# Optimization experiments

Hardware: AMD Instinct MI355X
Metric: run time of the kernel (lower is better)

Reference implementation:

```python
import jax, jax.numpy as jnp
import numpy as np

B, C, H, W = 64, 256, 14, 14
K = 9
HID = 256   # EdgeAgg hidden_channels = in_channels
OUT = 512   # out_channels = 2*in_channels (required by final reshape)


def _knn(q, kset, k):
    # ViG dense_knn_matrix: squared-distance knn, top-k of -dist (self-loop may be included)
    qs = jnp.sum(q * q, -1)
    ks = jnp.sum(kset * kset, -1)
    dist = qs[:, :, None] - 2.0 * jnp.einsum('bnc,bmc->bnm', q, kset) + ks[:, None, :]
    _, idx = jax.lax.top_k(-dist, k)   # (B,N,k) neighbor indices into kset
    return idx


def _edgeconv_add(feat, nbr, validf, w, b):
    # PyG EdgeConv(nn=Linear, aggr='add') with per-node valid-edge mask:
    #   out[i] = sum_{j in valid nbrs(i)} cat(x_i, x_j - x_i) @ w + b
    # nn is linear, so aggregate neighbor diffs BEFORE the matmul (same math, less traffic).
    Cf = feat.shape[-1]
    wa, wb = w[:Cf], w[Cf:]
    deg = jnp.sum(validf, -1, keepdims=True)                   # (B,N,1)
    xj = feat[jnp.arange(feat.shape[0])[:, None, None], nbr]   # (B,N,k,C) gather
    sum_xj = jnp.einsum('bnkc,bnk->bnc', xj, validf)
    return deg * (feat @ wa + b) + (sum_xj - deg * feat) @ wb


def _forward(x, fc1_w, fc1_b, fc2_w, fc2_b, fce_w, fce_b, inout_w, inout_b,
             attn_w, attn_b, upd_w, upd_b, kp_w, kp_b, enc_w, enc_b,
             mu_w, mu_b, dec_w, dec_b, T):
    k = dec_w.shape[-1]
    b_, c_, h_, w_ = x.shape
    n = h_ * w_
    xs = x.reshape(b_, c_, n)                       # (B,C,N)
    x_sp = jnp.transpose(xs, (0, 2, 1))             # (B,N,C) true spatial node feats for knn
    x_sp_d = jax.lax.stop_gradient(x_sp)            # original detaches before knn
    x_nbr = _knn(x_sp_d, x_sp_d, k)
    # temporal roll across the T frames of each clip
    y_sp = jnp.roll(x_sp.reshape(b_ // T, T, n, c_), -1, axis=1).reshape(b_, n, c_)
    y_nbr = _knn(x_sp_d, jax.lax.stop_gradient(y_sp), k)
    # faithful to original: x.view(B*N, C) reinterprets the contiguous (B,C,N) buffer
    x_feat = xs.reshape(b_, n, c_)
    y_feat = jnp.transpose(y_sp, (0, 2, 1)).reshape(b_, n, c_)
    # VAE-like K predictor (deterministic z = mu); argmax -> per-node degree in [0,k)
    hk = x_feat.reshape(b_ * n, c_) @ kp_w + kp_b
    hk = jax.nn.relu(hk @ enc_w + enc_b)
    mu = hk @ mu_w + mu_b
    logits = mu @ dec_w + dec_b                     # (B*N, k)
    k_int = jnp.argmax(logits, axis=1)
    # generate_mask: keep the first k_int[i] of node i's k edges
    validf = (jnp.arange(k)[None, :] < k_int[:, None]).astype(x.dtype).reshape(b_, n, k)

    def edge_agg(feat, nbr):
        h1 = jax.nn.relu(_edgeconv_add(feat, nbr, validf, fc1_w, fc1_b))
        h2 = _edgeconv_add(h1, nbr, validf, fc2_w, fc2_b)
        return (h2 @ fce_w + fce_b).reshape(b_ * n, -1)

    x_agg = edge_agg(x_feat, x_nbr)
    y_agg = edge_agg(y_feat, y_nbr)
    scores = (jnp.concatenate([x_agg, y_agg], -1) @ attn_w + attn_b)[:, 0]
    wgt = jax.nn.softmax(scores, axis=0)[:, None]   # softmax over ALL B*N nodes (as in source)
    fused = wgt * x_agg + (1.0 - wgt) * y_agg
    xin = x_feat.reshape(b_ * n, c_) @ inout_w + inout_b
    upd = jax.nn.relu(jnp.concatenate([xin, fused], -1) @ upd_w + upd_b)   # (B*N, 2C)
    return jnp.transpose(upd.reshape(b_, n, 2 * c_), (0, 2, 1)).reshape(b_, 2 * c_, h_, w_)


def setup_inputs():
    key = jax.random.key(0)
    ks = iter(jax.random.split(key, 32))

    def lin(i, o):
        return jax.random.normal(next(ks), (i, o), jnp.float32) / np.sqrt(i)

    def bias(o):
        return jax.random.normal(next(ks), (o,), jnp.float32) * 0.01

    return {
        'x': jax.random.normal(next(ks), (B, C, H, W), jnp.float32),
        'fc1_w': lin(2 * C, HID), 'fc1_b': bias(HID),
        'fc2_w': lin(2 * HID, HID), 'fc2_b': bias(HID),
        'fce_w': lin(HID, OUT), 'fce_b': bias(OUT),
        'inout_w': lin(C, OUT), 'inout_b': bias(OUT),
        'attn_w': lin(2 * OUT, 1), 'attn_b': bias(1),
        'upd_w': lin(2 * OUT, OUT), 'upd_b': bias(OUT),
        'kp_w': lin(C, 500), 'kp_b': bias(500),
        'enc_w': lin(500, 64), 'enc_b': bias(64),
        'mu_w': lin(64, 32), 'mu_b': bias(32),
        'dec_w': lin(32, K), 'dec_b': bias(K),
        'T': 16,
    }


def reference(x, fc1_w, fc1_b, fc2_w, fc2_b, fce_w, fce_b, inout_w, inout_b,
              attn_w, attn_b, upd_w, upd_b, kp_w, kp_b, enc_w, enc_b,
              mu_w, mu_b, dec_w, dec_b, T):
    return _forward(x, fc1_w, fc1_b, fc2_w, fc2_b, fce_w, fce_b, inout_w, inout_b,
                    attn_w, attn_b, upd_w, upd_b, kp_w, kp_b, enc_w, enc_b,
                    mu_w, mu_b, dec_w, dec_b, T)
```

## Files before the change

kernel.cpp:

```cpp
#include <hip/hip_runtime.h>
#include <cstddef>
#include <cstdint>

constexpr int BATCH = 64;
constexpr int CH    = 256;
constexpr int NPT   = 196;
constexpr int ROWS  = BATCH * NPT;
constexpr int BSTRIDE = CH * NPT;
constexpr int KNB   = 8;
constexpr int DSTR  = 208;

typedef __bf16 bf16x8 __attribute__((ext_vector_type(8)));
typedef __bf16 bf16x4 __attribute__((ext_vector_type(4)));
typedef _Float16 f16x8 __attribute__((ext_vector_type(8)));
typedef float  f32x4  __attribute__((ext_vector_type(4)));
typedef unsigned long long u64;

__device__ __forceinline__ int src_batch(int b) {
    return (b & ~15) | ((b + 1) & 15);
}

__device__ __forceinline__ void gload_lds16(const void* g, void* l) {
    __builtin_amdgcn_global_load_lds(
        (const __attribute__((address_space(1))) void*)g,
        (__attribute__((address_space(3))) void*)l, 16, 0, 0);
}

__device__ __forceinline__ int xcd_swz(int lin, int nwg) {
    int q = nwg >> 3;
    return (lin & 7) * q + (lin >> 3);
}

__global__ __launch_bounds__(256) void front_kernel(const float* __restrict__ x,
        _Float16* __restrict__ XH, _Float16* __restrict__ XL,
        __bf16* __restrict__ XB, float* __restrict__ qs,
        const float* __restrict__ fc1_w, const float* __restrict__ fc2_w,
        const float* __restrict__ fce_w, const float* __restrict__ upd_w,
        const float* __restrict__ kp_w, const float* __restrict__ kp_b,
        const float* __restrict__ enc_w, const float* __restrict__ enc_b,
        const float* __restrict__ mu_w, const float* __restrict__ mu_b,
        const float* __restrict__ dec_w, const float* __restrict__ dec_b,
        const float* __restrict__ inout_w, const float* __restrict__ inout_b,
        const float* __restrict__ upd_b,
        __bf16* __restrict__ W1catT, __bf16* __restrict__ W2catT,
        __bf16* __restrict__ fcet, __bf16* __restrict__ updC,
        float* __restrict__ KW1, float* __restrict__ kb1,
        float* __restrict__ KW2, float* __restrict__ kb2,
        float* __restrict__ bcomp, int* __restrict__ smcnt) {
    __shared__ __attribute__((aligned(16))) char smem[16896];
    float (*tile)[65] = (float(*)[65])smem;
    int bid = blockIdx.x;
    int t = threadIdx.x;
    if (bid < 1024) {
        int m0 = (bid & 3) * 64, c0 = ((bid >> 2) & 3) * 64, b = bid >> 4;
        const float* xb = x + (size_t)b * BSTRIDE;
        #pragma unroll
        for (int s = 0; s < 16; ++s) {
            int idx = s * 256 + t;
            int cc = idx >> 6, mm = idx & 63;
            int m = m0 + mm;
            float v = (m < NPT) ? xb[(size_t)(c0 + cc) * NPT + m] : 0.f;
            tile[cc][mm] = v;
            if (m < NPT)
                XB[(size_t)b * BSTRIDE + (size_t)(c0 + cc) * NPT + m] = (__bf16)v;
        }
        __syncthreads();
        #pragma unroll
        for (int s = 0; s < 16; ++s) {
            int idx = s * 256 + t;
            int mm = idx >> 6, cc = idx & 63;
            float v = tile[cc][mm];
            _Float16 h = (_Float16)v;
            size_t off = ((size_t)b * 256 + (m0 + mm)) * 256 + c0 + cc;
            XH[off] = h;
            XL[off] = (_Float16)(v - (float)h);
        }
    } else if (bid < 1088) {
        int b = bid - 1024;
        int m = t;
        if (m >= NPT) return;
        const float* xb = x + (size_t)b * BSTRIDE;
        float acc = 0.f;
        for (int c = 0; c < CH; ++c) {
            float v = xb[c * NPT + m];
            acc = fmaf(v, v, acc);
        }
        qs[b * NPT + m] = acc;
    } else {
        int pbid = bid - 1088;
        if (pbid == 0 && t == 0) smcnt[0] = 0;
        if (pbid < 64) {
            const float* W = (pbid < 32) ? fc1_w : fc2_w;
            __bf16* WT = (pbid < 32) ? W1catT : W2catT;
            int local = pbid & 31;
            int n0 = (local >> 2) * 64, k0 = (local & 3) * 64;
            #pragma unroll
            for (int s = 0; s < 16; ++s) {
                int idx = s * 256 + t;
                int kk = idx >> 6, nn = idx & 63;
                float v;
                if (n0 < 256)
                    v = W[(size_t)(k0 + kk) * 256 + n0 + nn] -
                        W[(size_t)(k0 + kk + 256) * 256 + n0 + nn];
                else
                    v = W[(size_t)(k0 + kk + 256) * 256 + (n0 - 256) + nn];
                tile[kk][nn] = v;
            }
            __syncthreads();
            #pragma unroll
            for (int s = 0; s < 16; ++s) {
                int idx = s * 256 + t;
                int nn = idx >> 6, kk = idx & 63;
                WT[(size_t)(n0 + nn) * 256 + k0 + kk] = (__bf16)tile[kk][nn];
            }
        } else if (pbid < 96) {
            int local = pbid - 64;
            int n0 = (local >> 2) * 64, k0 = (local & 3) * 64;
            #pragma unroll
            for (int s = 0; s < 16; ++s) {
                int idx = s * 256 + t;
                int kk = idx >> 6, nn = idx & 63;
                tile[kk][nn] = fce_w[(size_t)(k0 + kk) * 512 + n0 + nn];
            }
            __syncthreads();
            #pragma unroll
            for (int s = 0; s < 16; ++s) {
                int idx = s * 256 + t;
                int nn = idx >> 6, kk = idx & 63;
                fcet[(size_t)(n0 + nn) * 256 + k0 + kk] = (__bf16)tile[kk][nn];
            }
        } else if (pbid < 160) {
            int local = pbid - 96;
            int k0 = (local >> 3) * 64, n0 = (local & 7) * 64;
            #pragma unroll
            for (int s = 0; s < 16; ++s) {
                int idx = s * 256 + t;
                int kk = idx >> 6, nn = idx & 63;
                tile[kk][nn] = upd_w[(size_t)(512 + k0 + kk) * 512 + n0 + nn];
            }
            __syncthreads();
            #pragma unroll
            for (int s = 0; s < 16; ++s) {
                int idx = s * 256 + t;
                int nn = idx >> 6, kk = idx & 63;
                updC[(size_t)(n0 + nn) * 768 + 256 + k0 + kk] = (__bf16)tile[kk][nn];
            }
        } else if (pbid < 224) {
            int i = (pbid - 160) * 4 + (t >> 6);
            int j = t & 63;
            double acc = 0.0;
            for (int k = 0; k < 500; ++k)
                acc += (double)kp_w[(size_t)i * 500 + k] * (double)enc_w[(size_t)k * 64 + j];
            KW1[i * 64 + j] = (float)acc;
        } else if (pbid == 224) {
            int j = t;
            if (j < 64) {
                double acc = (double)enc_b[j];
                for (int k = 0; k < 500; ++k)
                    acc += (double)kp_b[k] * (double)enc_w[(size_t)k * 64 + j];
                kb1[j] = (float)acc;
            }
        } else if (pbid < 228) {
            int e = (pbid - 225) * 256 + t;
            if (e < 576) {
                int i = e / 9, j = e - (e / 9) * 9;
                double acc = 0.0;
                for (int k = 0; k < 32; ++k)
                    acc += (double)mu_w[(size_t)i * 32 + k] * (double)dec_w[(size_t)k * 9 + j];
                KW2[e] = (float)acc;
            } else if (e < 585) {
                int j = e - 576;
                double acc = (double)dec_b[j];
                for (int k = 0; k < 32; ++k)
                    acc += (double)mu_b[k] * (double)dec_w[(size_t)k * 9 + j];
                kb2[j] = (float)acc;
            }
        } else if (pbid < 356) {
            int k0 = (pbid - 228) * 2;
            int n = t;
            double a00 = 0.0, a01 = 0.0, a10 = 0.0, a11 = 0.0;
            const float* iw0 = inout_w + (size_t)k0 * 512;
            const float* iw1 = iw0 + 512;
            for (int j = 0; j < 512; ++j) {
                double u0 = (double)upd_w[(size_t)j * 512 + n];
                double u1 = (double)upd_w[(size_t)j * 512 + n + 256];
                double w0 = (double)iw0[j];
                double w1 = (double)iw1[j];
                a00 += w0 * u0; a01 += w0 * u1;
                a10 += w1 * u0; a11 += w1 * u1;
            }
            updC[(size_t)n * 768 + k0]           = (__bf16)(float)a00;
            updC[(size_t)(n + 256) * 768 + k0]   = (__bf16)(float)a01;
            updC[(size_t)n * 768 + k0 + 1]       = (__bf16)(float)a10;
            updC[(size_t)(n + 256) * 768 + k0 + 1] = (__bf16)(float)a11;
        } else {
            int n = (pbid - 356) * 256 + t;
            double acc = (double)upd_b[n];
            for (int j = 0; j < 512; ++j)
                acc += (double)inout_b[j] * (double)upd_w[(size_t)j * 512 + n];
            bcomp[n] = (float)acc;
        }
    }
}

__global__ __launch_bounds__(256) void gram_kint(const _Float16* __restrict__ XH,
        const _Float16* __restrict__ XL, const float* __restrict__ qs,
        float* __restrict__ Dw, const float* __restrict__ x,
        const float* __restrict__ W1, const float* __restrict__ b1,
        const float* __restrict__ W2, const float* __restrict__ b2,
        int* __restrict__ kint, float* __restrict__ degf) {
    __shared__ __attribute__((aligned(16))) char smem[21056];
    int bid = blockIdx.x;
    int t = threadIdx.x;
    if (bid < 2048) {
        _Float16* Ah = (_Float16*)smem;
        _Float16* Al = Ah + 2048;
        _Float16* Bh = Al + 2048;
        _Float16* Bl = Bh + 2048;
        int nid = xcd_swz(bid, 2048);
        int job = nid >> 4;
        int tile = nid & 15;
        int by = tile >> 2, bx = tile & 3;
        int r0 = by * 64, c0 = bx * 64;
        int qb = (job < 64) ? job : job - 64;
        int kb = (job < 64) ? qb : src_batch(qb);
        int w = t >> 6, l = t & 63;
        int lr = l & 15, lg = l >> 4;
        int wr = (w >> 1) * 32, wc = (w & 1) * 32;
        const _Float16* qh = XH + (size_t)qb * 65536;
        const _Float16* ql = XL + (size_t)qb * 65536;
        const _Float16* kh = XH + (size_t)kb * 65536;
        const _Float16* kl = XL + (size_t)kb * 65536;
        f32x4 acc[2][2] = {};
        for (int k0 = 0; k0 < 256; k0 += 32) {
            {
                int row = w * 16 + (l >> 2);
                int cb = (l & 3) * 8;
                size_t goA = (size_t)(r0 + row) * 256 + k0 + cb;
                size_t goB = (size_t)(c0 + row) * 256 + k0 + cb;
                gload_lds16(qh + goA, Ah + w * 512);
                gload_lds16(ql + goA, Al + w * 512);
                gload_lds16(kh + goB, Bh + w * 512);
                gload_lds16(kl + goB, Bl + w * 512);
            }
            asm volatile("s_waitcnt vmcnt(0)" ::: "memory");
            __syncthreads();
            f16x8 ah[2], alv[2], bh[2], blv[2];
            #pragma unroll
            for (int mi = 0; mi < 2; ++mi) {
                ah[mi]  = *(const f16x8*)(Ah + (wr + mi * 16 + lr) * 32 + lg * 8);
                alv[mi] = *(const f16x8*)(Al + (wr + mi * 16 + lr) * 32 + lg * 8);
            }
            #pragma unroll
            for (int ni = 0; ni < 2; ++ni) {
                bh[ni]  = *(const f16x8*)(Bh + (wc + ni * 16 + lr) * 32 + lg * 8);
                blv[ni] = *(const f16x8*)(Bl + (wc + ni * 16 + lr) * 32 + lg * 8);
            }
            #pragma unroll
            for (int mi = 0; mi < 2; ++mi)
                #pragma unroll
                for (int ni = 0; ni < 2; ++ni) {
                    acc[mi][ni] = __builtin_amdgcn_mfma_f32_16x16x32_f16(
                        ah[mi], bh[ni], acc[mi][ni], 0, 0, 0);
                    acc[mi][ni] = __builtin_amdgcn_mfma_f32_16x16x32_f16(
                        ah[mi], blv[ni], acc[mi][ni], 0, 0, 0);
                    acc[mi][ni] = __builtin_amdgcn_mfma_f32_16x16x32_f16(
                        alv[mi], bh[ni], acc[mi][ni], 0, 0, 0);
                }
            __syncthreads();
        }
        const float* qsq = qs + qb * NPT;
        const float* qsk = qs + kb * NPT;
        float ksv[2];
        #pragma unroll
        for (int ni = 0; ni < 2; ++ni) {
            int col = c0 + wc + ni * 16 + lr;
            ksv[ni] = (col < NPT) ? qsk[col] : 0.f;
        }
        #pragma unroll
        for (int mi = 0; mi < 2; ++mi) {
            #pragma unroll
            for (int r = 0; r < 4; ++r) {
                if (r0 + wr + mi * 16 + r >= NPT) continue;
                int grow = r0 + wr + mi * 16 + lg * 4 + r;
                if (grow >= NPT) continue;
                float qq = qsq[grow];
                size_t rbase = ((size_t)job * NPT + grow) * DSTR;
                #pragma unroll
                for (int ni = 0; ni < 2; ++ni) {
                    int col = c0 + wc + ni * 16 + lr;
                    if (col < NPT)
                        Dw[rbase + col] = qq - 2.f * acc[mi][ni][r] + ksv[ni];
                }
            }
        }
    } else {
        float (*xr)[256] = (float(*)[256])smem;
        float (*ebuf)[64] = (float(*)[64])(smem + 16384);
        float (*lg2)[9]  = (float(*)[9])(smem + 20480);
        int r0 = (bid - 2048) * 16;
        const float4* xg = (const float4*)(x + (size_t)r0 * 256);
        float4* xs = (float4*)&xr[0][0];
        #pragma unroll
        for (int s = 0; s < 4; ++s) xs[s * 256 + t] = xg[s * 256 + t];
        __syncthreads();
        int w = t >> 6, l = t & 63;
        {
            float bb = b1[l];
            float a0 = bb, a1 = bb, a2 = bb, a3 = bb;
            const float* x0 = xr[w * 4 + 0];
            const float* x1 = xr[w * 4 + 1];
            const float* x2 = xr[w * 4 + 2];
            const float* x3 = xr[w * 4 + 3];
            for (int c = 0; c < 256; ++c) {
                float wv = W1[c * 64 + l];
                a0 = fmaf(x0[c], wv, a0);
                a1 = fmaf(x1[c], wv, a1);
                a2 = fmaf(x2[c], wv, a2);
                a3 = fmaf(x3[c], wv, a3);
            }
            ebuf[w * 4 + 0][l] = fmaxf(a0, 0.f);
            ebuf[w * 4 + 1][l] = fmaxf(a1, 0.f);
            ebuf[w * 4 + 2][l] = fmaxf(a2, 0.f);
            ebuf[w * 4 + 3][l] = fmaxf(a3, 0.f);
        }
        __syncthreads();
        int rr = t >> 4, cc = t & 15;
        if (cc < 9) {
            float acc = b2[cc];
            for (int j = 0; j < 64; ++j)
                acc = fmaf(ebuf[rr][j], W2[j * 9 + cc], acc);
            lg2[rr][cc] = acc;
        }
        __syncthreads();
        if (cc == 0) {
            float best = lg2[rr][0];
            int bi = 0;
            #pragma unroll
            for (int j = 1; j < 9; ++j)
                if (lg2[rr][j] > best) { best = lg2[rr][j]; bi = j; }
            kint[r0 + rr] = bi;
            degf[r0 + rr] = (float)bi;
        }
    }
}

__global__ __launch_bounds__(256) void topk_p1(const float* __restrict__ Dw,
        int* __restrict__ nbr, const __bf16* __restrict__ XB,
        const __bf16* __restrict__ W1catT, __bf16* __restrict__ P1) {
    __shared__ __attribute__((aligned(16))) char smem[32768];
    int bid = blockIdx.x;
    int t = threadIdx.x;
    if (bid < 392) {
        u64 (*lists)[4][8] = (u64(*)[4][8])smem;
        int lrow = t >> 2, q = t & 3;
        int rowid = bid * 64 + lrow;
        const float* rp = Dw + (size_t)rowid * DSTR + q * 52;
        u64 kreg[8];
        #pragma unroll
        for (int p = 0; p < 8; ++p) kreg[p] = ~0ull;
        for (int s4 = 0; s4 < 13; ++s4) {
            f32x4 dv = *(const f32x4*)(rp + s4 * 4);
            #pragma unroll
            for (int e = 0; e < 4; ++e) {
                int col = q * 52 + s4 * 4 + e;
                unsigned u = __float_as_uint(dv[e]);
                u = (u & 0x80000000u) ? ~u : (u | 0x80000000u);
                u64 key = (col < NPT) ? (((u64)u << 32) | (unsigned)col) : ~0ull;
                if (key < kreg[7]) {
                    #pragma unroll
                    for (int p = 0; p < 8; ++p) {
                        u64 mn = (key < kreg[p]) ? key : kreg[p];
                        u64 mx = (key < kreg[p]) ? kreg[p] : key;
                        kreg[p] = mn; key = mx;
                    }
                }
            }
        }
        #pragma unroll
        for (int p = 0; p < 8; ++p) lists[lrow][q][p] = kreg[p];
        __syncthreads();
        if (q == 0) {
            const u64* c = &lists[lrow][0][0];
            int p0 = 0, p1 = 0, p2 = 0, p3 = 0;
            #pragma unroll
            for (int it = 0; it < 8; ++it) {
                u64 v0 = c[p0], v1 = c[8 + p1], v2 = c[16 + p2], v3 = c[24 + p3];
                u64 best = v0; int bj = 0;
                if (v1 < best) { best = v1; bj = 1; }
                if (v2 < best) { best = v2; bj = 2; }
                if (v3 < best) { best = v3; bj = 3; }
                if (bj == 0) p0 = (p0 < 7) ? p0 + 1 : 7;
                else if (bj == 1) p1 = (p1 < 7) ? p1 + 1 : 7;
                else if (bj == 2) p2 = (p2 < 7) ? p2 + 1 : 7;
                else p3 = (p3 < 7) ? p3 + 1 : 7;
                nbr[(size_t)rowid * KNB + it] = (int)(best & 0xffffffffu);
            }
        }
    } else {
        __bf16* As = (__bf16*)smem;
        __bf16* Bs = As + 128 * 64;
        int lin = bid - 392;
        int nid = xcd_swz(lin, 392);
        int bx = nid & 3, by = nid >> 2;
        int w = t >> 6, l = t & 63;
        int r0 = by * 128, c0 = bx * 128;
        int lr = l & 15, lg = l >> 4;
        int wr = (w >> 1) * 64, wc = (w & 1) * 64;
        constexpr int K = 256, N = 512;
        f32x4 acc[4][4] = {};
        for (int k0 = 0; k0 < K; k0 += 64) {
            #pragma unroll
            for (int i = 0; i < 4; ++i) {
                int row = (w * 4 + i) * 8 + (l >> 3);
                int c8 = l & 7;
                gload_lds16(XB + (size_t)(r0 + row) * K + k0 + c8 * 8,
                            As + (w * 4 + i) * 512);
                gload_lds16(W1catT + (size_t)(c0 + row) * K + k0 + c8 * 8,
                            Bs + (w * 4 + i) * 512);
            }
            asm volatile("s_waitcnt vmcnt(0)" ::: "memory");
            __syncthreads();
            #pragma unroll
            for (int ks = 0; ks < 2; ++ks) {
                bf16x8 af[4], bfr[4];
                #pragma unroll
                for (int mi = 0; mi < 4; ++mi)
                    af[mi] = *(const bf16x8*)(As + (wr + mi * 16 + lr) * 64 + ks * 32 + lg * 8);
                #pragma unroll
                for (int ni = 0; ni < 4; ++ni)
                    bfr[ni] = *(const bf16x8*)(Bs + (wc + ni * 16 + lr) * 64 + ks * 32 + lg * 8);
                #pragma unroll
                for (int mi = 0; mi < 4; ++mi)
                    #pragma unroll
                    for (int ni = 0; ni < 4; ++ni)
                        acc[mi][ni] = __builtin_amdgcn_mfma_f32_16x16x32_bf16(
                            af[mi], bfr[ni], acc[mi][ni], 0, 0, 0);
            }
            __syncthreads();
        }
        #pragma unroll
        for (int mi = 0; mi < 4; ++mi) {
            #pragma unroll
            for (int r = 0; r < 4; ++r) {
                int row = r0 + wr + mi * 16 + lg * 4 + r;
                #pragma unroll
                for (int ni = 0; ni < 4; ++ni) {
                    int col = c0 + wc + ni * 16 + lr;
                    P1[(size_t)row * N + col] = (__bf16)acc[mi][ni][r];
                }
            }
        }
    }
}

template<int STAGE, int RELU>
__global__ __launch_bounds__(256) void combine_kernel(const __bf16* __restrict__ P,
        const int* __restrict__ nbr, const int* __restrict__ kint_,
        const float* __restrict__ degf, const float* __restrict__ bias,
        __bf16* __restrict__ H) {
    int g = threadIdx.x >> 6, lane = threadIdx.x & 63;
    int nid = xcd_swz(blockIdx.x, 2 * ROWS / 4);
    int r = nid * 4 + g;
    int branch = (r >= ROWS);
    int rr = r - branch * ROWS;
    int b = rr / NPT, i = rr - b * NPT;
    size_t srow, mbase;
    if constexpr (STAGE == 1) {
        int fb = branch ? src_batch(b) : b;
        srow = (size_t)fb * NPT + i;
        mbase = (size_t)fb * NPT;
    } else {
        srow = (size_t)r;
        mbase = (size_t)branch * ROWS + (size_t)b * NPT;
    }
    const int* nb = nbr + (size_t)branch * ((size_t)ROWS * KNB) + (size_t)rr * KNB;
    bf16x4 sv = *(const bf16x4*)(P + srow * 512 + lane * 4);
    float4 bv = *(const float4*)(bias + lane * 4);
    float s0 = 0.f, s1 = 0.f, s2 = 0.f, s3 = 0.f;
    int kk = kint_[rr];
    for (int tt = 0; tt < kk; ++tt) {
        int m = nb[tt];
        bf16x4 v = *(const bf16x4*)(P + (mbase + m) * 512 + 256 + lane * 4);
        s0 += (float)v[0]; s1 += (float)v[1]; s2 += (float)v[2]; s3 += (float)v[3];
    }
    float dg = degf[rr];
    float o0 = fmaf(dg, (float)sv[0] + bv.x, s0);
    float o1 = fmaf(dg, (float)sv[1] + bv.y, s1);
    float o2 = fmaf(dg, (float)sv[2] + bv.z, s2);
    float o3 = fmaf(dg, (float)sv[3] + bv.w, s3);
    if constexpr (RELU) {
        o0 = fmaxf(o0, 0.f); o1 = fmaxf(o1, 0.f);
        o2 = fmaxf(o2, 0.f); o3 = fmaxf(o3, 0.f);
    }
    bf16x4 ov;
    ov[0] = (__bf16)o0; ov[1] = (__bf16)o1; ov[2] = (__bf16)o2; ov[3] = (__bf16)o3;
    *(bf16x4*)(H + (size_t)r * 256 + lane * 4) = ov;
}

template<int FLAGS, int CONCAT>
__global__ __launch_bounds__(256) void mfma_gemm(
    const __bf16* __restrict__ A0, const __bf16* __restrict__ A1,
    const __bf16* __restrict__ WT, const float* __restrict__ bias,
    float* __restrict__ Cf, __bf16* __restrict__ Cb, int K, int N,
    const float* __restrict__ aw, float* __restrict__ scp,
    const float* __restrict__ wgt) {
    constexpr int SMEMB = (FLAGS & 8) ? (128 * 129 * 4) : (2 * 128 * 64 * 2);
    __shared__ __attribute__((aligned(16))) char smem[SMEMB];
    __bf16* As = (__bf16*)smem;
    __bf16* Bs = As + 128 * 64;
    int lin = blockIdx.x + 4 * blockIdx.y;
    int nid = xcd_swz(lin, 4 * gridDim.y);
    int bx = nid & 3, by = nid >> 2;
    int t = threadIdx.x, w = t >> 6, l = t & 63;
    int r0 = by * 128, c0 = bx * 128;
    int lr = l & 15, lg = l >> 4;
    int wr = (w >> 1) * 64, wc = (w & 1) * 64;
    f32x4 acc[4][4] = {};
    for (int k0 = 0; k0 < K; k0 += 64) {
        #pragma unroll
        for (int i = 0; i < 4; ++i) {
            int row = (w * 4 + i) * 8 + (l >> 3);
            int c8 = l & 7;
            if constexpr (CONCAT == 2) {
                if (k0 < 256) {
                    gload_lds16(A0 + (size_t)(r0 + row) * 256 + k0 + c8 * 8,
                                As + (w * 4 + i) * 512);
                } else {
                    int kk2 = k0 - 256 + c8 * 8;
                    size_t gr = (size_t)(r0 + row);
                    bf16x8 xa = *(const bf16x8*)(A1 + gr * 512 + kk2);
                    bf16x8 ya = *(const bf16x8*)(A1 + ((size_t)ROWS + gr) * 512 + kk2);
                    float wv = wgt[gr];
                    bf16x8 mx;
                    #pragma unroll
                    for (int j = 0; j < 8; ++j)
                        mx[j] = (__bf16)(wv * (float)xa[j] + (1.f - wv) * (float)ya[j]);
                    *(bf16x8*)(As + (w * 4 + i) * 512 + l * 8) = mx;
                }
            } else {
                gload_lds16(A0 + (size_t)(r0 + row) * K + k0 + c8 * 8,
                            As + (w * 4 + i) * 512);
            }
            gload_lds16(WT + (size_t)(c0 + row) * K + k0 + c8 * 8,
                        Bs + (w * 4 + i) * 512);
        }
        asm volatile("s_waitcnt vmcnt(0)" ::: "memory");
        __syncthreads();
        #pragma unroll
        for (int ks = 0; ks < 2; ++ks) {
            bf16x8 af[4], bfr[4];
            #pragma unroll
            for (int mi = 0; mi < 4; ++mi)
                af[mi] = *(const bf16x8*)(As + (wr + mi * 16 + lr) * 64 + ks * 32 + lg * 8);
            #pragma unroll
            for (int ni = 0; ni < 4; ++ni)
                bfr[ni] = *(const bf16x8*)(Bs + (wc + ni * 16 + lr) * 64 + ks * 32 + lg * 8);
            #pragma unroll
            for (int mi = 0; mi < 4; ++mi)
                #pragma unroll
                for (int ni = 0; ni < 4; ++ni)
                    acc[mi][ni] = __builtin_amdgcn_mfma_f32_16x16x32_bf16(
                        af[mi], bfr[ni], acc[mi][ni], 0, 0, 0);
        }
        __syncthreads();
    }
    if constexpr ((FLAGS & 8) != 0) {
        float* tile = (float*)smem;
        #pragma unroll
        for (int mi = 0; mi < 4; ++mi)
            #pragma unroll
            for (int r = 0; r < 4; ++r) {
                int rrow = wr + mi * 16 + lg * 4 + r;
                #pragma unroll
                for (int ni = 0; ni < 4; ++ni) {
                    int ccol = wc + ni * 16 + lr;
                    float v = acc[mi][ni][r];
                    if (bias) v += bias[c0 + ccol];
                    if constexpr ((FLAGS & 1) != 0) v = fmaxf(v, 0.f);
                    tile[rrow * 129 + ccol] = v;
                }
            }
        __syncthreads();
        int cc = t >> 6, rr2 = t & 63;
        #pragma unroll
        for (int cs = 0; cs < 128; cs += 4) {
            #pragma unroll
            for (int h = 0; h < 2; ++h) {
                int row = r0 + rr2 + h * 64;
                int bb = row / NPT, ii = row - bb * NPT;
                Cf[((size_t)bb * 512 + (c0 + cc + cs)) * NPT + ii] =
                    tile[(rr2 + h * 64) * 129 + cc + cs];
            }
        }
    } else if constexpr ((FLAGS & 16) != 0) {
        int half = (r0 >= ROWS) ? 1 : 0;
        float ps[4][4] = {};
        #pragma unroll
        for (int mi = 0; mi < 4; ++mi)
            #pragma unroll
            for (int r = 0; r < 4; ++r) {
                int row = r0 + wr + mi * 16 + lg * 4 + r;
                #pragma unroll
                for (int ni = 0; ni < 4; ++ni) {
                    int col = c0 + wc + ni * 16 + lr;
                    float v = acc[mi][ni][r] + bias[col];
                    Cb[(size_t)row * N + col] = (__bf16)v;
                    ps[mi][r] = fmaf(v, aw[half * 512 + col], ps[mi][r]);
                }
            }
        #pragma unroll
        for (int m = 1; m <= 8; m <<= 1)
            #pragma unroll
            for (int mi = 0; mi < 4; ++mi)
                #pragma unroll
                for (int r = 0; r < 4; ++r)
                    ps[mi][r] += __shfl_xor(ps[mi][r], m, 64);
        if (lr == 0) {
            int slot = half * 8 + bx * 2 + (w & 1);
            #pragma unroll
            for (int mi = 0; mi < 4; ++mi)
                #pragma unroll
                for (int r = 0; r < 4; ++r) {
                    int sr = r0 - half * ROWS + wr + mi * 16 + lg * 4 + r;
                    scp[(size_t)slot * ROWS + sr] = ps[mi][r];
                }
        }
    } else {
        #pragma unroll
        for (int mi = 0; mi < 4; ++mi) {
            #pragma unroll
            for (int r = 0; r < 4; ++r) {
                int row = r0 + wr + mi * 16 + lg * 4 + r;
                #pragma unroll
                for (int ni = 0; ni < 4; ++ni) {
                    int col = c0 + wc + ni * 16 + lr;
                    float v = acc[mi][ni][r];
                    if (bias) v += bias[col];
                    if constexpr ((FLAGS & 1) != 0) v = fmaxf(v, 0.f);
                    if constexpr ((FLAGS & 4) != 0)
                        Cb[(size_t)row * N + col] = (__bf16)v;
                    else
                        Cf[(size_t)row * N + col] = v;
                }
            }
        }
    }
}

__global__ __launch_bounds__(256) void softmax_all(const float* __restrict__ scp,
        const float* __restrict__ ab, float* __restrict__ scores,
        float* __restrict__ mpart, float* __restrict__ spart,
        int* __restrict__ cnt, float* __restrict__ wgt) {
    __shared__ float red[256];
    __shared__ float MS[2];
    __shared__ bool islast;
    int t = threadIdx.x;
    int sr = blockIdx.x * 256 + t;
    float s = ab[0];
    #pragma unroll
    for (int i = 0; i < 16; ++i) s += scp[(size_t)i * ROWS + sr];
    scores[sr] = s;
    red[t] = s; __syncthreads();
    for (int off = 128; off; off >>= 1) {
        if (t < off) red[t] = fmaxf(red[t], red[t + off]);
        __syncthreads();
    }
    float mb = red[0]; __syncthreads();
    red[t] = expf(s - mb); __syncthreads();
    for (int off = 128; off; off >>= 1) {
        if (t < off) red[t] += red[t + off];
        __syncthreads();
    }
    if (t == 0) {
        mpart[blockIdx.x] = mb;
        spart[blockIdx.x] = red[0];
        __threadfence();
        int old = atomicAdd(cnt, 1);
        islast = (old == 48);
    }
    __syncthreads();
    if (!islast) return;
    __threadfence();
    if (t == 0) {
        float M = mpart[0];
        for (int i = 1; i < 49; ++i) M = fmaxf(M, mpart[i]);
        float S = 0.f;
        for (int i = 0; i < 49; ++i) S += spart[i] * expf(mpart[i] - M);
        MS[0] = M; MS[1] = S;
        cnt[0] = 0;
    }
    __syncthreads();
    float M = MS[0], denom = MS[1];
    for (int i = t; i < ROWS; i += 256)
        wgt[i] = expf(scores[i] - M) / denom;
}

extern "C" void kernel_launch(void* const* d_in, const int* in_sizes, int n_in,
                              void* d_out, int out_size, void* d_ws, size_t ws_size,
                              hipStream_t stream) {
    (void)in_sizes; (void)n_in; (void)out_size; (void)ws_size;
    const float* x       = (const float*)d_in[0];
    const float* fc1_w   = (const float*)d_in[1];
    const float* fc1_b   = (const float*)d_in[2];
    const float* fc2_w   = (const float*)d_in[3];
    const float* fc2_b   = (const float*)d_in[4];
    const float* fce_w   = (const float*)d_in[5];
    const float* fce_b   = (const float*)d_in[6];
    const float* inout_w = (const float*)d_in[7];
    const float* inout_b = (const float*)d_in[8];
    const float* attn_w  = (const float*)d_in[9];
    const float* attn_b  = (const float*)d_in[10];
    const float* upd_w   = (const float*)d_in[11];
    const float* upd_b   = (const float*)d_in[12];
    const float* kp_w    = (const float*)d_in[13];
    const float* kp_b    = (const float*)d_in[14];
    const float* enc_w   = (const float*)d_in[15];
    const float* enc_b   = (const float*)d_in[16];
    const float* mu_w    = (const float*)d_in[17];
    const float* mu_b    = (const float*)d_in[18];
    const float* dec_w   = (const float*)d_in[19];
    const float* dec_b   = (const float*)d_in[20];
    float* out = (float*)d_out;

    char* base = (char*)d_ws;
    size_t o = 0;
    auto alloc = [&](size_t bytes) -> void* {
        void* p = base + o;
        o += (bytes + 255) & ~(size_t)255;
        return p;
    };
    float* qs     = (float*)alloc(ROWS * 4);
    float* degf   = (float*)alloc(ROWS * 4);
    float* scores = (float*)alloc(ROWS * 4);
    float* wgt    = (float*)alloc(ROWS * 4);
    int*   kint   = (int*)  alloc(ROWS * 4);
    float* KW1    = (float*)alloc(256 * 64 * 4);
    float* kb1    = (float*)alloc(64 * 4);
    float* KW2    = (float*)alloc(64 * 9 * 4);
    float* kb2    = (float*)alloc(9 * 4);
    float* bcomp  = (float*)alloc(512 * 4);
    float* scp    = (float*)alloc((size_t)16 * ROWS * 4);
    float* mpart  = (float*)alloc(64 * 4);
    float* spart  = (float*)alloc(64 * 4);
    int*   smcnt  = (int*)  alloc(256);
    int*   nbr    = (int*)  alloc((size_t)128 * NPT * KNB * 4);
    char*  regD   = (char*) alloc((size_t)ROWS * 512 * 2);
    __bf16* XB    = (__bf16*)alloc((size_t)ROWS * 256 * 2);
    __bf16* H1    = (__bf16*)alloc((size_t)2 * ROWS * 256 * 2);
    __bf16* H2    = (__bf16*)alloc((size_t)2 * ROWS * 256 * 2);
    char*  regAGG = (char*) alloc((size_t)2 * ROWS * 512 * 4);
    __bf16* W1catT= (__bf16*)alloc((size_t)512 * 256 * 2);
    __bf16* W2catT= (__bf16*)alloc((size_t)512 * 256 * 2);
    __bf16* fcet  = (__bf16*)alloc((size_t)512 * 256 * 2);
    __bf16* updC  = (__bf16*)alloc((size_t)512 * 768 * 2);
    __bf16* P1buf = (__bf16*)regD;
    _Float16* XSPH = (_Float16*)regAGG;
    _Float16* XSPL = XSPH + (size_t)64 * 256 * 256;
    float* Dw     = (float*)(regAGG + (size_t)17 * 1024 * 1024);
    __bf16* P2buf = (__bf16*)regAGG;
    __bf16* AGGb  = (__bf16*)regAGG;
    __bf16* XAGGb = AGGb;

    front_kernel<<<1446, 256, 0, stream>>>(x, XSPH, XSPL, XB, qs,
                                           fc1_w, fc2_w, fce_w, upd_w,
                                           kp_w, kp_b, enc_w, enc_b,
                                           mu_w, mu_b, dec_w, dec_b,
                                           inout_w, inout_b, upd_b,
                                           W1catT, W2catT, fcet, updC,
                                           KW1, kb1, KW2, kb2, bcomp, smcnt);

    gram_kint<<<2832, 256, 0, stream>>>(XSPH, XSPL, qs, Dw, x,
                                        KW1, kb1, KW2, kb2, kint, degf);

    topk_p1<<<784, 256, 0, stream>>>(Dw, nbr, XB, W1catT, P1buf);

    combine_kernel<1, 1><<<2 * ROWS / 4, 256, 0, stream>>>(
        P1buf, nbr, kint, degf, fc1_b, H1);

    mfma_gemm<4, 0><<<dim3(4, 196), 256, 0, stream>>>(
        H1, nullptr, W2catT, nullptr, nullptr, P2buf, 256, 512,
        nullptr, nullptr, nullptr);
    combine_kernel<2, 0><<<2 * ROWS / 4, 256, 0, stream>>>(
        P2buf, nbr, kint, degf, fc2_b, H2);

    mfma_gemm<20, 0><<<dim3(4, 196), 256, 0, stream>>>(
        H2, nullptr, fcet, fce_b, nullptr, AGGb, 256, 512,
        attn_w, scp, nullptr);

    softmax_all<<<49, 256, 0, stream>>>(scp, attn_b, scores, mpart, spart,
                                        smcnt, wgt);

    mfma_gemm<9, 2><<<dim3(4, 98), 256, 0, stream>>>(
        XB, XAGGb, updC, bcomp, out, nullptr, 768, 512,
        nullptr, nullptr, wgt);
}
```

Before: 230.8 us.

## Fuse squared norms into transpose, split updC precompute, double-buffer gram loads

The squared-norm computation moves out of its own 64 blocks and into the transpose blocks, which already hold each tile in LDS; they write four per-channel-chunk partials that the gram kernel sums. The updC weight-product precompute is spread over 512 blocks with one output per thread instead of 128 blocks with four outputs each, to shorten the long serial tail in front_kernel. The gram kernel's LDS staging is double-buffered, so the next k-slice loads while MFMA runs on the current one. Costs are more LDS per block (which may lower occupancy), more blocks in the front kernel, and four partial reads per norm lookup.

```diff
diff --git a/kernel.cpp b/kernel.cpp
--- a/kernel.cpp
+++ b/kernel.cpp
@@ -33,7 +33,7 @@
 
 __global__ __launch_bounds__(256) void front_kernel(const float* __restrict__ x,
         _Float16* __restrict__ XH, _Float16* __restrict__ XL,
-        __bf16* __restrict__ XB, float* __restrict__ qs,
+        __bf16* __restrict__ XB, float* __restrict__ qsp,
         const float* __restrict__ fc1_w, const float* __restrict__ fc2_w,
         const float* __restrict__ fce_w, const float* __restrict__ upd_w,
         const float* __restrict__ kp_w, const float* __restrict__ kp_b,
@@ -75,19 +75,17 @@
             XH[off] = h;
             XL[off] = (_Float16)(v - (float)h);
         }
-    } else if (bid < 1088) {
-        int b = bid - 1024;
-        int m = t;
-        if (m >= NPT) return;
-        const float* xb = x + (size_t)b * BSTRIDE;
-        float acc = 0.f;
-        for (int c = 0; c < CH; ++c) {
-            float v = xb[c * NPT + m];
-            acc = fmaf(v, v, acc);
-        }
-        qs[b * NPT + m] = acc;
+        if (t < 64) {
+            float acc = 0.f;
+            #pragma unroll
+            for (int cc = 0; cc < 64; ++cc) {
+                float v = tile[cc][t];
+                acc = fmaf(v, v, acc);
+            }
+            qsp[(size_t)(c0 >> 6) * 16384 + b * 256 + m0 + t] = acc;
+        }
     } else {
-        int pbid = bid - 1088;
+        int pbid = bid - 1024;
         if (pbid == 0 && t == 0) smcnt[0] = 0;
         if (pbid < 64) {
             const float* W = (pbid < 32) ? fc1_w : fc2_w;
@@ -175,26 +173,15 @@
                     acc += (double)mu_b[k] * (double)dec_w[(size_t)k * 9 + j];
                 kb2[j] = (float)acc;
             }
-        } else if (pbid < 356) {
-            int k0 = (pbid - 228) * 2;
-            int n = t;
-            double a00 = 0.0, a01 = 0.0, a10 = 0.0, a11 = 0.0;
-            const float* iw0 = inout_w + (size_t)k0 * 512;
-            const float* iw1 = iw0 + 512;
-            for (int j = 0; j < 512; ++j) {
-                double u0 = (double)upd_w[(size_t)j * 512 + n];
-                double u1 = (double)upd_w[(size_t)j * 512 + n + 256];
-                double w0 = (double)iw0[j];
-                double w1 = (double)iw1[j];
-                a00 += w0 * u0; a01 += w0 * u1;
-                a10 += w1 * u0; a11 += w1 * u1;
-            }
-            updC[(size_t)n * 768 + k0]           = (__bf16)(float)a00;
-            updC[(size_t)(n + 256) * 768 + k0]   = (__bf16)(float)a01;
-            updC[(size_t)n * 768 + k0 + 1]       = (__bf16)(float)a10;
-            updC[(size_t)(n + 256) * 768 + k0 + 1] = (__bf16)(float)a11;
+        } else if (pbid < 740) {
+            int e = (pbid - 228) * 256 + t;
+            int k = e >> 9, n = e & 511;
+            double acc = 0.0;
+            for (int j = 0; j < 512; ++j)
+                acc += (double)inout_w[(size_t)k * 512 + j] * (double)upd_w[(size_t)j * 512 + n];
+            updC[(size_t)n * 768 + k] = (__bf16)(float)acc;
         } else {
-            int n = (pbid - 356) * 256 + t;
+            int n = (pbid - 740) * 256 + t;
             double acc = (double)upd_b[n];
             for (int j = 0; j < 512; ++j)
                 acc += (double)inout_b[j] * (double)upd_w[(size_t)j * 512 + n];
@@ -204,19 +191,15 @@
 }
 
 __global__ __launch_bounds__(256) void gram_kint(const _Float16* __restrict__ XH,
-        const _Float16* __restrict__ XL, const float* __restrict__ qs,
+        const _Float16* __restrict__ XL, const float* __restrict__ qsp,
         float* __restrict__ Dw, const float* __restrict__ x,
         const float* __restrict__ W1, const float* __restrict__ b1,
         const float* __restrict__ W2, const float* __restrict__ b2,
         int* __restrict__ kint, float* __restrict__ degf) {
-    __shared__ __attribute__((aligned(16))) char smem[21056];
+    __shared__ __attribute__((aligned(16))) char smem[32768];
     int bid = blockIdx.x;
     int t = threadIdx.x;
     if (bid < 2048) {
-        _Float16* Ah = (_Float16*)smem;
-        _Float16* Al = Ah + 2048;
-        _Float16* Bh = Al + 2048;
-        _Float16* Bl = Bh + 2048;
         int nid = xcd_swz(bid, 2048);
         int job = nid >> 4;
         int tile = nid & 15;
@@ -231,20 +214,33 @@
         const _Float16* ql = XL + (size_t)qb * 65536;
         const _Float16* kh = XH + (size_t)kb * 65536;
         const _Float16* kl = XL + (size_t)kb * 65536;
+        int srow = w * 16 + (l >> 2);
+        int scb = (l & 3) * 8;
         f32x4 acc[2][2] = {};
-        for (int k0 = 0; k0 < 256; k0 += 32) {
-            {
-                int row = w * 16 + (l >> 2);
-                int cb = (l & 3) * 8;
-                size_t goA = (size_t)(r0 + row) * 256 + k0 + cb;
-                size_t goB = (size_t)(c0 + row) * 256 + k0 + cb;
-                gload_lds16(qh + goA, Ah + w * 512);
-                gload_lds16(ql + goA, Al + w * 512);
-                gload_lds16(kh + goB, Bh + w * 512);
-                gload_lds16(kl + goB, Bl + w * 512);
-            }
-            asm volatile("s_waitcnt vmcnt(0)" ::: "memory");
+        auto stage = [&](int k0, int bsel) {
+            _Float16* base = (_Float16*)(smem + bsel * 16384);
+            size_t goA = (size_t)(r0 + srow) * 256 + k0 + scb;
+            size_t goB = (size_t)(c0 + srow) * 256 + k0 + scb;
+            gload_lds16(qh + goA, base + w * 512);
+            gload_lds16(ql + goA, base + 2048 + w * 512);
+            gload_lds16(kh + goB, base + 4096 + w * 512);
+            gload_lds16(kl + goB, base + 6144 + w * 512);
+        };
+        stage(0, 0);
+        #pragma unroll
+        for (int ks8 = 0; ks8 < 8; ++ks8) {
+            if (ks8 < 7) {
+                stage((ks8 + 1) * 32, (ks8 + 1) & 1);
+                asm volatile("s_waitcnt vmcnt(4)" ::: "memory");
+            } else {
+                asm volatile("s_waitcnt vmcnt(0)" ::: "memory");
+            }
             __syncthreads();
+            _Float16* base = (_Float16*)(smem + (ks8 & 1) * 16384);
+            _Float16* Ah = base;
+            _Float16* Al = base + 2048;
+            _Float16* Bh = base + 4096;
+            _Float16* Bl = base + 6144;
             f16x8 ah[2], alv[2], bh[2], blv[2];
             #pragma unroll
             for (int mi = 0; mi < 2; ++mi) {
@@ -269,13 +265,15 @@
                 }
             __syncthreads();
         }
-        const float* qsq = qs + qb * NPT;
-        const float* qsk = qs + kb * NPT;
         float ksv[2];
         #pragma unroll
         for (int ni = 0; ni < 2; ++ni) {
             int col = c0 + wc + ni * 16 + lr;
-            ksv[ni] = (col < NPT) ? qsk[col] : 0.f;
+            if (col < NPT) {
+                size_t o0 = (size_t)kb * 256 + col;
+                ksv[ni] = ((qsp[o0] + qsp[16384 + o0]) + qsp[32768 + o0]) +
+                          qsp[49152 + o0];
+            } else ksv[ni] = 0.f;
         }
         #pragma unroll
         for (int mi = 0; mi < 2; ++mi) {
@@ -284,7 +282,9 @@
                 if (r0 + wr + mi * 16 + r >= NPT) continue;
                 int grow = r0 + wr + mi * 16 + lg * 4 + r;
                 if (grow >= NPT) continue;
-                float qq = qsq[grow];
+                size_t o0 = (size_t)qb * 256 + grow;
+                float qq = ((qsp[o0] + qsp[16384 + o0]) + qsp[32768 + o0]) +
+                           qsp[49152 + o0];
                 size_t rbase = ((size_t)job * NPT + grow) * DSTR;
                 #pragma unroll
                 for (int ni = 0; ni < 2; ++ni) {
@@ -730,7 +730,7 @@
         o += (bytes + 255) & ~(size_t)255;
         return p;
     };
-    float* qs     = (float*)alloc(ROWS * 4);
+    float* qsp    = (float*)alloc((size_t)4 * 64 * 256 * 4);
     float* degf   = (float*)alloc(ROWS * 4);
     float* scores = (float*)alloc(ROWS * 4);
     float* wgt    = (float*)alloc(ROWS * 4);
@@ -762,7 +762,7 @@
     __bf16* AGGb  = (__bf16*)regAGG;
     __bf16* XAGGb = AGGb;
 
-    front_kernel<<<1446, 256, 0, stream>>>(x, XSPH, XSPL, XB, qs,
+    front_kernel<<<1766, 256, 0, stream>>>(x, XSPH, XSPL, XB, qsp,
                                            fc1_w, fc2_w, fce_w, upd_w,
                                            kp_w, kp_b, enc_w, enc_b,
                                            mu_w, mu_b, dec_w, dec_b,
@@ -770,7 +770,7 @@
                                            W1catT, W2catT, fcet, updC,
                                            KW1, kb1, KW2, kb2, bcomp, smcnt);
 
-    gram_kint<<<2832, 256, 0, stream>>>(XSPH, XSPL, qs, Dw, x,
+    gram_kint<<<2832, 256, 0, stream>>>(XSPH, XSPL, qsp, Dw, x,
                                         KW1, kb1, KW2, kb2, kint, degf);
 
     topk_p1<<<784, 256, 0, stream>>>(Dw, nbr, XB, W1catT, P1buf);
```

New measurement: 210.7 us. 1.1x faster.
